# Kernel optimization log

Measured on AMD Instinct MI355X. Metric: run time of the kernel, lower is better.

## Reference

```python
import jax, jax.numpy as jnp
import numpy as np
from jax import lax

B, T, H, F, K, M, NB = 32, 1024, 256, 256, 3, 4096, 256


def setup_inputs() -> dict:
    key = jax.random.key(0)
    ks = jax.random.split(key, 10)
    s = 0.05
    inp = {}
    inp["x"] = jax.random.normal(ks[0], (B, T, H), jnp.float32)
    inp["src_mask"] = jnp.zeros((B, T), bool)
    inp["duration_target"] = jax.random.randint(ks[1], (B, T), 0, 7)
    inp["pitch_target"] = jax.random.uniform(ks[2], (B, T), jnp.float32)
    inp["energy_target"] = jax.random.uniform(ks[3], (B, T), jnp.float32)
    inp["max_len"] = M
    # stacked params for 3 predictors: [duration, pitch, energy]
    inp["w1"] = jax.random.normal(ks[4], (3, K, H, F), jnp.float32) * s  # WIO layout
    inp["b1"] = jnp.zeros((3, F), jnp.float32)
    inp["g1"] = jnp.ones((3, F), jnp.float32)
    inp["be1"] = jnp.zeros((3, F), jnp.float32)
    inp["w2"] = jax.random.normal(ks[5], (3, K, F, F), jnp.float32) * s
    inp["b2"] = jnp.zeros((3, F), jnp.float32)
    inp["g2"] = jnp.ones((3, F), jnp.float32)
    inp["be2"] = jnp.zeros((3, F), jnp.float32)
    inp["lw"] = jax.random.normal(ks[6], (3, F, 1), jnp.float32) * s
    inp["lb"] = jnp.zeros((3, 1), jnp.float32)
    inp["pitch_bins"] = jnp.linspace(0.0, 1.0, NB - 1, dtype=jnp.float32)
    inp["pitch_emb"] = jax.random.normal(ks[7], (NB, H), jnp.float32) * 0.1
    inp["energy_bins"] = jnp.linspace(0.0, 1.0, NB - 1, dtype=jnp.float32)
    inp["energy_emb"] = jax.random.normal(ks[8], (NB, H), jnp.float32) * 0.1
    return inp


def _conv_relu_ln(x, w, b, g, be):
    # Conv1d (k=3, pad=1) over seq dim with channels-last, then ReLU, then LayerNorm.
    h = lax.conv_general_dilated(x, w, (1,), [(1, 1)],
                                 dimension_numbers=('NWC', 'WIO', 'NWC'))
    h = jax.nn.relu(h + b)
    mu = jnp.mean(h, -1, keepdims=True)
    var = jnp.var(h, -1, keepdims=True)
    return (h - mu) * lax.rsqrt(var + 1e-5) * g + be


def _predictor(x, i, w1, b1, g1, be1, w2, b2, g2, be2, lw, lb, mask):
    h = _conv_relu_ln(x, w1[i], b1[i], g1[i], be1[i])
    h = _conv_relu_ln(h, w2[i], b2[i], g2[i], be2[i])
    out = (h @ lw[i] + lb[i])[..., 0]  # [B, T]
    return jnp.where(mask, 0.0, out)


def _length_regulate(x, dur, max_len):
    # vectorized version of the per-sample repeat/cat/pad LengthRegulator
    cum = jnp.cumsum(dur, axis=1)                     # [B, T]
    mel_len = jnp.minimum(cum[:, -1], max_len)        # [B]
    frames = jnp.arange(max_len)                      # [M]
    # frame j maps to phoneme i with cum[i-1] <= j < cum[i]
    idx = jax.vmap(lambda c: jnp.searchsorted(c, frames, side='right'))(cum)
    idx = jnp.minimum(idx, x.shape[1] - 1)
    out = jnp.take_along_axis(x, idx[:, :, None], axis=1)  # [B, M, H]
    valid = frames[None, :] < mel_len[:, None]
    return out * valid[:, :, None].astype(x.dtype), mel_len, ~valid


def reference(x, src_mask, duration_target, pitch_target, energy_target, max_len,
              w1, b1, g1, be1, w2, b2, g2, be2, lw, lb,
              pitch_bins, pitch_emb, energy_bins, energy_emb):
    P = (w1, b1, g1, be1, w2, b2, g2, be2, lw, lb)
    # predictor_grad = 1.0 -> x.detach() + 1.0*(x - x.detach()) == x
    log_dur = _predictor(x, 0, *P, src_mask)
    pitch_pred = _predictor(x, 1, *P, src_mask)
    p_e = pitch_emb[jnp.searchsorted(pitch_bins, pitch_target, side='left')]
    energy_pred = _predictor(x, 2, *P, src_mask)
    e_e = energy_emb[jnp.searchsorted(energy_bins, energy_target, side='left')]
    output = x + p_e + e_e
    out, mel_len, mel_mask = _length_regulate(output, duration_target, max_len)
    return (out, pitch_pred, energy_pred, log_dur, duration_target, mel_len, mel_mask)
```

## Files before the change

kernel.cpp:

```cpp
#include <hip/hip_runtime.h>
#include <hip/hip_bf16.h>
#include <stdint.h>


typedef __bf16 bf16;
typedef __attribute__((ext_vector_type(8))) __bf16 bf16x8;
typedef __attribute__((ext_vector_type(4))) float f32x4;

#define TSEQ 1024

#define O1 33554432
#define O2 33587200
#define O3 33619968
#define O4 33652736
#define O5 33685504
#define O6 33685536

#define OUT_END_B 135266432

#define XB_OFF 512
#define H1B_OFF (XB_OFF + 16777216)
#define H1B_SZ 16777216
#define WT_OFF (H1B_OFF + 3 * H1B_SZ)
#define WT_SZ 393216

#define XB_SZ 16777216
#define H1B_TOT (3 * H1B_SZ)
#define WT_TOT (6 * WT_SZ)
#define SCRATCH_SZ (XB_SZ + H1B_TOT + WT_TOT)

#define CUM_OFF 0
#define ADDROW_OFF 131072
#define ZEROS_OFF 262144
#define WS_SCR_OFF 524288
#define WS_NEED ((size_t)WS_SCR_OFF + (size_t)SCRATCH_SZ)

__global__ __launch_bounds__(256) void k_prep(
    const float* __restrict__ x, bf16* __restrict__ xb,
    const float* __restrict__ w1, const float* __restrict__ w2,
    bf16* __restrict__ wt,
    const float* __restrict__ pt, const float* __restrict__ et,
    const float* __restrict__ pbins, const float* __restrict__ ebins,
    int* __restrict__ addrow, float* __restrict__ zpage,
    const int* __restrict__ dur, const int* __restrict__ maxlen,
    float* __restrict__ out, int* __restrict__ cum) {
  int bid = blockIdx.x;
  int tid = threadIdx.x;
  if (bid < 4096) {
    int t = bid * 256 + tid;
    int g = t >> 5;
    int u = t & 31;
    const float4* s = (const float4*)(x + ((size_t)g << 8) + (u << 3));
    float4 a = s[0], b = s[1];
    bf16x8 o;
    o[0] = (bf16)a.x; o[1] = (bf16)a.y; o[2] = (bf16)a.z; o[3] = (bf16)a.w;
    o[4] = (bf16)b.x; o[5] = (bf16)b.y; o[6] = (bf16)b.z; o[7] = (bf16)b.w;
    *(bf16x8*)(xb + ((size_t)g << 8) + (u << 3)) = o;
  } else if (bid < 4672) {
    int bw = bid - 4096;
    int m = bw / 96;
    int r = bw % 96;
    int f = (r & 3) * 64 + (tid & 63);
    int u = (r >> 2) * 4 + (tid >> 6);
    const float* W = (m < 3) ? w1 : w2;
    int i = (m < 3) ? m : m - 3;
    int dt = u >> 5;
    int c0 = (u & 31) << 3;
    const float* src = W + (((size_t)(i * 3 + dt) * 256 + c0) << 8) + f;
    bf16x8 o;
#pragma unroll
    for (int cc = 0; cc < 8; ++cc) o[cc] = (bf16)src[(size_t)cc << 8];
    *(bf16x8*)(wt + (size_t)m * 196608 + (size_t)f * 768 + (u << 3)) = o;
  } else if (bid < 4800) {
    __shared__ float pb[255], eb[255];
    if (tid < 255) { pb[tid] = pbins[tid]; eb[tid] = ebins[tid]; }
    if (bid == 4672 && tid < 64) zpage[tid] = 0.f;
    __syncthreads();
    int g = (bid - 4672) * 256 + tid;
    float pv = pt[g], ev = et[g];
    int lo = 0, hi = 255;
    while (lo < hi) { int md = (lo + hi) >> 1; if (pb[md] < pv) lo = md + 1; else hi = md; }
    int pi = lo;
    lo = 0; hi = 255;
    while (lo < hi) { int md = (lo + hi) >> 1; if (eb[md] < ev) lo = md + 1; else hi = md; }
    addrow[g] = pi | (lo << 16);
  } else {
    __shared__ int lds[256];
    int b = bid - 4800;
    int4 d = ((const int4*)(dur + b * 1024))[tid];
    int p0 = d.x, p1 = p0 + d.y, p2 = p1 + d.z, p3 = p2 + d.w;
    int val = p3;
    lds[tid] = val;
    __syncthreads();
    for (int off = 1; off < 256; off <<= 1) {
      int t = (tid >= off) ? lds[tid - off] : 0;
      __syncthreads();
      val += t;
      lds[tid] = val;
      __syncthreads();
    }
    int excl = val - p3;
    int4 c;
    c.x = excl + p0; c.y = excl + p1; c.z = excl + p2; c.w = excl + p3;
    ((int4*)(cum + b * 1024))[tid] = c;
    float4 fd;
    fd.x = (float)d.x; fd.y = (float)d.y; fd.z = (float)d.z; fd.w = (float)d.w;
    ((float4*)(out + O4 + b * 1024))[tid] = fd;
    if (tid == 255) {
      int mel = val < maxlen[0] ? val : maxlen[0];
      out[O5 + b] = (float)mel;
    }
  }
}

__global__ __launch_bounds__(256, 2) void k_conv(
    const char* __restrict__ Ab, size_t AperY, const char* __restrict__ Wb,
    const float* __restrict__ bias0, const float* __restrict__ gamma0,
    const float* __restrict__ beta0, char* __restrict__ hout0,
    const float* __restrict__ lw0, const float* __restrict__ lb0,
    const unsigned char* __restrict__ mask, float* __restrict__ outb,
    const char* __restrict__ zpage, int mode,
    const float* __restrict__ xf, const int* __restrict__ cum,
    const int* __restrict__ addrow, const float* __restrict__ pemb,
    const float* __restrict__ eemb, const int* __restrict__ maxlen,
    int lrbase) {
  __shared__ __align__(16) char Abuf[3][8192];
  __shared__ __align__(16) char Bbuf[3][16384];
  __shared__ float redS[128][2];
  __shared__ float redS2[128][2];
  __shared__ float predr[128][2];

  const int tid = threadIdx.x;
  const int bid = blockIdx.x;

  if (bid >= 768) {
    int* cl = (int*)Abuf;
    int rid0 = lrbase + ((bid - 768) << 4);
    int b = rid0 >> 12;
    ((int4*)cl)[tid] = ((const int4*)(cum + (b << 10)))[tid];
    __syncthreads();
    int lane = tid & 63;
    int wv = tid >> 6;
    int total = cl[1023];
    int ml = maxlen[0];
    int mel = total < ml ? total : ml;
    int c1 = cl[lane * 16 + 15];
#pragma unroll
    for (int rr = 0; rr < 4; ++rr) {
      int rid = rid0 + (wv << 2) + rr;
      int j = rid & 4095;
      bool valid = j < mel;
      float4 res = {0.f, 0.f, 0.f, 0.f};
      if (valid) {
        unsigned long long m1 = __ballot(j < c1);
        int s = __ffsll(m1) - 1;
        unsigned long long m2 = __ballot(j < cl[s * 16 + (lane & 15)]);
        int p = __ffsll(m2) - 1;
        int i = s * 16 + p;
        int ar = addrow[(b << 10) + i];
        int pi = ar & 0xffff, ei = ar >> 16;
        const float4* xr = (const float4*)(xf + (((size_t)(b << 10) + i) << 8));
        const float4* pr = (const float4*)(pemb + ((size_t)pi << 8));
        const float4* er = (const float4*)(eemb + ((size_t)ei << 8));
        float4 a = xr[lane], pp = pr[lane], e = er[lane];
        res.x = a.x + pp.x + e.x;
        res.y = a.y + pp.y + e.y;
        res.z = a.z + pp.z + e.z;
        res.w = a.w + pp.w + e.w;
      }
      ((float4*)(outb + ((size_t)rid << 8)))[lane] = res;
      if (lane == 0) outb[O6 + rid] = valid ? 0.f : 1.f;
    }
    return;
  }

  const int wv = tid >> 6;
  const int ln = tid & 63;
  const int q = ln >> 4;
  const int m16 = ln & 15;
  const int rh = wv >> 1;
  const int ch = wv & 1;
  const int y = bid >> 8;
  const int g0 = (bid & 255) << 7;
  const int t0 = g0 & (TSEQ - 1);

  const char* A = Ab + (size_t)y * AperY;
  const char* W = Wb + (size_t)y * WT_SZ;

  const int srow = ln >> 2;
  const int slot = ln & 3;
  const int usw = slot ^ ((ln >> 3) & 3);

  const char* bsrc[4];
#pragma unroll
  for (int j = 0; j < 4; ++j) {
    int f = j * 64 + wv * 16 + srow;
    bsrc[j] = W + ((size_t)f * 768 + usw * 8) * 2;
  }
  const int rbase = wv * 16 + srow;

  f32x4 acc[4][8];
#pragma unroll
  for (int a = 0; a < 4; a++)
#pragma unroll
    for (int b = 0; b < 8; b++) acc[a][b] = (f32x4){0.f, 0.f, 0.f, 0.f};

#define STAGE(KB, BUF)                                                         \
  {                                                                            \
    int dt0_ = (KB) >> 3;                                                      \
    int c0_ = ((KB) & 7) << 5;                                                 \
    char* ad_ = Abuf[BUF];                                                     \
    char* bd_ = Bbuf[BUF];                                                     \
    _Pragma("unroll") for (int j = 0; j < 2; ++j) {                            \
      int rr = j * 64 + rbase + dt0_ - 1;                                      \
      const char* src = ((unsigned)(t0 + rr) < 1024u)                          \
          ? A + (((size_t)(g0 + rr) << 8) + c0_ + usw * 8) * 2                 \
          : zpage + slot * 16;                                                 \
      __builtin_amdgcn_global_load_lds(                                        \
          (const __attribute__((address_space(1))) void*)src,                  \
          (__attribute__((address_space(3))) void*)(ad_ + j * 4096 +           \
                                                    tid * 16),                 \
          16, 0, 0);                                                           \
    }                                                                          \
    _Pragma("unroll") for (int j = 0; j < 4; ++j) {                            \
      __builtin_amdgcn_global_load_lds(                                        \
          (const __attribute__((address_space(1))) void*)(bsrc[j] + (KB)*64),  \
          (__attribute__((address_space(3))) void*)(bd_ + j * 4096 +           \
                                                    tid * 16),                 \
          16, 0, 0);                                                           \
    }                                                                          \
  }

  const int spq = (q ^ ((m16 >> 1) & 3)) << 4;
  const int aoff = (rh * 64 + m16) * 64 + spq;
  const int boff = (ch * 128 + m16) * 64 + spq;

  STAGE(0, 0);
  STAGE(1, 1);
  int cur = 0, stg = 2;
  for (int kb = 0; kb < 24; ++kb) {
    if (kb < 23)
      asm volatile("s_waitcnt vmcnt(6)" ::: "memory");
    else
      asm volatile("s_waitcnt vmcnt(0)" ::: "memory");
    __builtin_amdgcn_s_barrier();
    if (kb < 22) STAGE(kb + 2, stg);
    const char* Ac = Abuf[cur];
    const char* Bc = Bbuf[cur];
    bf16x8 af[4], bfr[8];
#pragma unroll
    for (int mi = 0; mi < 4; ++mi)
      af[mi] = *(const bf16x8*)(Ac + aoff + mi * 1024);
#pragma unroll
    for (int ni = 0; ni < 8; ++ni)
      bfr[ni] = *(const bf16x8*)(Bc + boff + ni * 1024);
    __builtin_amdgcn_s_setprio(1);
#pragma unroll
    for (int mi = 0; mi < 4; ++mi)
#pragma unroll
      for (int ni = 0; ni < 8; ++ni)
        acc[mi][ni] = __builtin_amdgcn_mfma_f32_16x16x32_bf16(
            af[mi], bfr[ni], acc[mi][ni], 0, 0, 0);
    __builtin_amdgcn_s_setprio(0);
    asm volatile("s_waitcnt lgkmcnt(0)" ::: "memory");
    cur = (cur == 2) ? 0 : cur + 1;
    stg = (stg == 2) ? 0 : stg + 1;
  }
#undef STAGE

  const float* bias = bias0 + y * 256;
  const float* gamma = gamma0 + y * 256;
  const float* beta = beta0 + y * 256;
  float bias_v[8], g_v[8], be_v[8], lw_v[8];
#pragma unroll
  for (int ni = 0; ni < 8; ni++) {
    int nf = (ch << 7) + (ni << 4) + m16;
    bias_v[ni] = bias[nf];
    g_v[ni] = gamma[nf];
    be_v[ni] = beta[nf];
  }
  if (mode) {
    const float* lw = lw0 + y * 256;
#pragma unroll
    for (int ni = 0; ni < 8; ni++) lw_v[ni] = lw[(ch << 7) + (ni << 4) + m16];
  }

#pragma unroll
  for (int mi = 0; mi < 4; mi++) {
#pragma unroll
    for (int r = 0; r < 4; r++) {
      float s1 = 0.f, s2 = 0.f;
#pragma unroll
      for (int ni = 0; ni < 8; ni++) {
        float v = acc[mi][ni][r] + bias_v[ni];
        v = fmaxf(v, 0.f);
        acc[mi][ni][r] = v;
        s1 += v;
        s2 += v * v;
      }
#pragma unroll
      for (int d = 1; d < 16; d <<= 1) {
        s1 += __shfl_xor(s1, d);
        s2 += __shfl_xor(s2, d);
      }
      if (m16 == 0) {
        int m = (rh << 6) + (mi << 4) + (q << 2) + r;
        redS[m][ch] = s1;
        redS2[m][ch] = s2;
      }
    }
  }
  __syncthreads();

  if (mode == 0) {
    bf16* hp = (bf16*)(hout0 + (size_t)y * H1B_SZ);
#pragma unroll
    for (int mi = 0; mi < 4; mi++) {
#pragma unroll
      for (int r = 0; r < 4; r++) {
        int m = (rh << 6) + (mi << 4) + (q << 2) + r;
        float mu = (redS[m][0] + redS[m][1]) * 0.00390625f;
        float var = (redS2[m][0] + redS2[m][1]) * 0.00390625f - mu * mu;
        float rs = rsqrtf(var + 1e-5f);
        int gg = g0 + m;
#pragma unroll
        for (int ni = 0; ni < 8; ni++) {
          float v = (acc[mi][ni][r] - mu) * rs * g_v[ni] + be_v[ni];
          int n = (ch << 7) + (ni << 4) + m16;
          hp[((size_t)gg << 8) + n] = (bf16)v;
        }
      }
    }
  } else {
#pragma unroll
    for (int mi = 0; mi < 4; mi++) {
#pragma unroll
      for (int r = 0; r < 4; r++) {
        int m = (rh << 6) + (mi << 4) + (q << 2) + r;
        float mu = (redS[m][0] + redS[m][1]) * 0.00390625f;
        float var = (redS2[m][0] + redS2[m][1]) * 0.00390625f - mu * mu;
        float rs = rsqrtf(var + 1e-5f);
        float p = 0.f;
#pragma unroll
        for (int ni = 0; ni < 8; ni++) {
          float v = (acc[mi][ni][r] - mu) * rs * g_v[ni] + be_v[ni];
          p += v * lw_v[ni];
        }
#pragma unroll
        for (int d = 1; d < 16; d <<= 1) p += __shfl_xor(p, d);
        if (m16 == 0) predr[m][ch] = p;
      }
    }
    __syncthreads();
    if (tid < 128) {
      int gg = g0 + tid;
      float p = predr[tid][0] + predr[tid][1] + lb0[y];
      if (mask[gg]) p = 0.f;
      float* pd = outb + (y == 0 ? O3 : (y == 1 ? O1 : O2));
      pd[gg] = p;
    }
  }
}

__global__ __launch_bounds__(256) void k_lr(const float* __restrict__ x,
                                            const int* __restrict__ cum,
                                            const int* __restrict__ addrow,
                                            const float* __restrict__ pemb,
                                            const float* __restrict__ eemb,
                                            const int* __restrict__ maxlen,
                                            float* __restrict__ outb) {
  __shared__ int cl[1024];
  int tid = threadIdx.x;
  int rid0 = blockIdx.x << 4;
  int b = rid0 >> 12;
  ((int4*)cl)[tid] = ((const int4*)(cum + (b << 10)))[tid];
  __syncthreads();
  int lane = tid & 63;
  int wv = tid >> 6;
  int total = cl[1023];
  int ml = maxlen[0];
  int mel = total < ml ? total : ml;
  int c1 = cl[lane * 16 + 15];
#pragma unroll
  for (int rr = 0; rr < 4; ++rr) {
    int rid = rid0 + (wv << 2) + rr;
    int j = rid & 4095;
    bool valid = j < mel;
    float4 res = {0.f, 0.f, 0.f, 0.f};
    if (valid) {
      unsigned long long m1 = __ballot(j < c1);
      int s = __ffsll(m1) - 1;
      unsigned long long m2 = __ballot(j < cl[s * 16 + (lane & 15)]);
      int p = __ffsll(m2) - 1;
      int i = s * 16 + p;
      int ar = addrow[(b << 10) + i];
      int pi = ar & 0xffff, ei = ar >> 16;
      const float4* xr = (const float4*)(x + (((size_t)(b << 10) + i) << 8));
      const float4* pr = (const float4*)(pemb + ((size_t)pi << 8));
      const float4* er = (const float4*)(eemb + ((size_t)ei << 8));
      float4 a = xr[lane], pp = pr[lane], e = er[lane];
      res.x = a.x + pp.x + e.x;
      res.y = a.y + pp.y + e.y;
      res.z = a.z + pp.z + e.z;
      res.w = a.w + pp.w + e.w;
    }
    ((float4*)(outb + ((size_t)rid << 8)))[lane] = res;
    if (lane == 0) outb[O6 + rid] = valid ? 0.f : 1.f;
  }
}

extern "C" void kernel_launch(void* const* d_in, const int* in_sizes, int n_in,
                              void* d_out, int out_size, void* d_ws, size_t ws_size,
                              hipStream_t stream) {
  const float* x = (const float*)d_in[0];
  const unsigned char* src_mask = (const unsigned char*)d_in[1];
  const int* dur = (const int*)d_in[2];
  const float* pt = (const float*)d_in[3];
  const float* et = (const float*)d_in[4];
  const int* maxlen = (const int*)d_in[5];
  const float* w1 = (const float*)d_in[6];
  const float* b1 = (const float*)d_in[7];
  const float* g1 = (const float*)d_in[8];
  const float* be1 = (const float*)d_in[9];
  const float* w2 = (const float*)d_in[10];
  const float* b2 = (const float*)d_in[11];
  const float* g2 = (const float*)d_in[12];
  const float* be2 = (const float*)d_in[13];
  const float* lw = (const float*)d_in[14];
  const float* lb = (const float*)d_in[15];
  const float* pbins = (const float*)d_in[16];
  const float* pemb = (const float*)d_in[17];
  const float* ebins = (const float*)d_in[18];
  const float* eemb = (const float*)d_in[19];

  float* outf = (float*)d_out;
  char* ob = (char*)d_out;
  int* cum = (int*)((char*)d_ws + CUM_OFF);
  int* addrow = (int*)((char*)d_ws + ADDROW_OFF);
  float* zpage = (float*)((char*)d_ws + ZEROS_OFF);

  int merged = 0;
  char* sb = nullptr;
  if (ws_size >= WS_NEED) {
    sb = (char*)d_ws + WS_SCR_OFF;
    merged = 1;
  } else if ((size_t)out_size >= (size_t)OUT_END_B + (size_t)SCRATCH_SZ) {
    sb = ob + OUT_END_B;
    merged = 1;
  }
  bf16* xb;
  char* h1b;
  bf16* wt;
  if (merged) {
    xb = (bf16*)sb;
    h1b = sb + XB_SZ;
    wt = (bf16*)(sb + XB_SZ + H1B_TOT);
  } else {
    xb = (bf16*)(ob + XB_OFF);
    h1b = ob + H1B_OFF;
    wt = (bf16*)(ob + WT_OFF);
  }

  hipLaunchKernelGGL(k_prep, dim3(4832), dim3(256), 0, stream,
                     x, xb, w1, w2, wt, pt, et, pbins, ebins, addrow, zpage,
                     dur, maxlen, outf, cum);

  int gconv = merged ? 768 + 4096 : 768;
  hipLaunchKernelGGL(k_conv, dim3(gconv), dim3(256), 0, stream,
                     (const char*)xb, (size_t)0, (const char*)wt, b1, g1, be1,
                     h1b, lw, lb, src_mask, outf, (const char*)zpage, 0,
                     x, cum, addrow, pemb, eemb, maxlen, 0);
  hipLaunchKernelGGL(k_conv, dim3(gconv), dim3(256), 0, stream,
                     (const char*)h1b, (size_t)H1B_SZ,
                     (const char*)wt + 3 * WT_SZ, b2, g2, be2,
                     (char*)nullptr, lw, lb, src_mask, outf,
                     (const char*)zpage, 1,
                     x, cum, addrow, pemb, eemb, maxlen, 65536);
  if (!merged) {
    hipLaunchKernelGGL(k_lr, dim3(8192), dim3(256), 0, stream, x, cum, addrow,
                       pemb, eemb, maxlen, outf);
  }
}
```

Before: 330.2 us.

## Enlarge conv GEMM tile to 256 rows with 512-thread blocks

The conv kernel now uses 512-thread blocks, each computing a 256-row by 256-channel tile with 2x4 warp tiling instead of 128 rows with 2x2 warps. Each staged weight slice is reused across twice as many rows, halving weight reloads, and the LayerNorm reduction scratch is aliased into the A staging buffer. The grid halves, so fewer blocks run concurrently. The per-iteration lgkmcnt wait is removed and the main loop is unrolled by three. The risks are higher LDS use, fewer waves in flight, and possible register pressure from 512 threads at two blocks per CU.

```diff
diff --git a/kernel.cpp b/kernel.cpp
--- a/kernel.cpp
+++ b/kernel.cpp
@@ -113,7 +113,7 @@
   }
 }
 
-__global__ __launch_bounds__(256, 2) void k_conv(
+__global__ __launch_bounds__(512, 2) void k_conv(
     const char* __restrict__ Ab, size_t AperY, const char* __restrict__ Wb,
     const float* __restrict__ bias0, const float* __restrict__ gamma0,
     const float* __restrict__ beta0, char* __restrict__ hout0,
@@ -124,20 +124,20 @@
     const int* __restrict__ addrow, const float* __restrict__ pemb,
     const float* __restrict__ eemb, const int* __restrict__ maxlen,
     int lrbase) {
-  __shared__ __align__(16) char Abuf[3][8192];
-  __shared__ __align__(16) char Bbuf[3][16384];
-  __shared__ float redS[128][2];
-  __shared__ float redS2[128][2];
-  __shared__ float predr[128][2];
+  __shared__ __align__(16) char Ab3[3][16384];
+  __shared__ __align__(16) char Bb3[3][16384];
+  float (*redS)[4] = (float(*)[4])((char*)Ab3);
+  float (*redS2)[4] = (float(*)[4])((char*)Ab3 + 4096);
+  float (*predr)[4] = (float(*)[4])((char*)Ab3 + 8192);
 
   const int tid = threadIdx.x;
   const int bid = blockIdx.x;
 
-  if (bid >= 768) {
-    int* cl = (int*)Abuf;
-    int rid0 = lrbase + ((bid - 768) << 4);
+  if (bid >= 384) {
+    int* cl = (int*)Ab3;
+    int rid0 = lrbase + ((bid - 384) << 5);
     int b = rid0 >> 12;
-    ((int4*)cl)[tid] = ((const int4*)(cum + (b << 10)))[tid];
+    if (tid < 256) ((int4*)cl)[tid] = ((const int4*)(cum + (b << 10)))[tid];
     __syncthreads();
     int lane = tid & 63;
     int wv = tid >> 6;
@@ -178,91 +178,90 @@
   const int ln = tid & 63;
   const int q = ln >> 4;
   const int m16 = ln & 15;
-  const int rh = wv >> 1;
-  const int ch = wv & 1;
-  const int y = bid >> 8;
-  const int g0 = (bid & 255) << 7;
+  const int wm = wv >> 2;
+  const int wn = wv & 3;
+  const int y = bid >> 7;
+  const int g0 = (bid & 127) << 8;
   const int t0 = g0 & (TSEQ - 1);
 
   const char* A = Ab + (size_t)y * AperY;
   const char* W = Wb + (size_t)y * WT_SZ;
 
-  const int srow = ln >> 2;
-  const int slot = ln & 3;
-  const int usw = slot ^ ((ln >> 3) & 3);
-
-  const char* bsrc[4];
-#pragma unroll
-  for (int j = 0; j < 4; ++j) {
-    int f = j * 64 + wv * 16 + srow;
-    bsrc[j] = W + ((size_t)f * 768 + usw * 8) * 2;
-  }
-  const int rbase = wv * 16 + srow;
-
-  f32x4 acc[4][8];
-#pragma unroll
-  for (int a = 0; a < 4; a++)
-#pragma unroll
-    for (int b = 0; b < 8; b++) acc[a][b] = (f32x4){0.f, 0.f, 0.f, 0.f};
+  const int slot = tid & 3;
+  const int chunk = slot ^ ((tid >> 3) & 3);
+
+  const char* bsrc[2];
+#pragma unroll
+  for (int j = 0; j < 2; ++j) {
+    int f = j * 128 + (tid >> 2);
+    bsrc[j] = W + ((size_t)f * 768 + chunk * 8) * 2;
+  }
+
+  f32x4 acc[8][4];
+#pragma unroll
+  for (int a = 0; a < 8; a++)
+#pragma unroll
+    for (int b = 0; b < 4; b++) acc[a][b] = (f32x4){0.f, 0.f, 0.f, 0.f};
 
 #define STAGE(KB, BUF)                                                         \
   {                                                                            \
-    int dt0_ = (KB) >> 3;                                                      \
-    int c0_ = ((KB) & 7) << 5;                                                 \
-    char* ad_ = Abuf[BUF];                                                     \
-    char* bd_ = Bbuf[BUF];                                                     \
+    int dt_ = (KB) >> 3;                                                       \
+    int c0_ = ((KB)&7) << 5;                                                   \
+    char* ad_ = Ab3[BUF];                                                      \
+    char* bd_ = Bb3[BUF];                                                      \
     _Pragma("unroll") for (int j = 0; j < 2; ++j) {                            \
-      int rr = j * 64 + rbase + dt0_ - 1;                                      \
-      const char* src = ((unsigned)(t0 + rr) < 1024u)                          \
-          ? A + (((size_t)(g0 + rr) << 8) + c0_ + usw * 8) * 2                 \
+      int rowv = j * 128 + (tid >> 2);                                         \
+      int trow = t0 - 1 + rowv + dt_;                                          \
+      const char* src = ((unsigned)trow < 1024u)                               \
+          ? A + (((size_t)(g0 - 1 + rowv + dt_) << 8) + c0_ + chunk * 8) * 2   \
           : zpage + slot * 16;                                                 \
       __builtin_amdgcn_global_load_lds(                                        \
           (const __attribute__((address_space(1))) void*)src,                  \
-          (__attribute__((address_space(3))) void*)(ad_ + j * 4096 +           \
+          (__attribute__((address_space(3))) void*)(ad_ + j * 8192 +           \
                                                     tid * 16),                 \
           16, 0, 0);                                                           \
     }                                                                          \
-    _Pragma("unroll") for (int j = 0; j < 4; ++j) {                            \
+    _Pragma("unroll") for (int j = 0; j < 2; ++j) {                            \
       __builtin_amdgcn_global_load_lds(                                        \
           (const __attribute__((address_space(1))) void*)(bsrc[j] + (KB)*64),  \
-          (__attribute__((address_space(3))) void*)(bd_ + j * 4096 +           \
+          (__attribute__((address_space(3))) void*)(bd_ + j * 8192 +           \
                                                     tid * 16),                 \
           16, 0, 0);                                                           \
     }                                                                          \
   }
 
   const int spq = (q ^ ((m16 >> 1) & 3)) << 4;
-  const int aoff = (rh * 64 + m16) * 64 + spq;
-  const int boff = (ch * 128 + m16) * 64 + spq;
+  const int abase = (wm * 128 + m16) * 64 + spq;
+  const int bbase = (wn * 64 + m16) * 64 + spq;
 
   STAGE(0, 0);
   STAGE(1, 1);
   int cur = 0, stg = 2;
+#pragma unroll 3
   for (int kb = 0; kb < 24; ++kb) {
     if (kb < 23)
-      asm volatile("s_waitcnt vmcnt(6)" ::: "memory");
+      asm volatile("s_waitcnt vmcnt(4)" ::: "memory");
     else
       asm volatile("s_waitcnt vmcnt(0)" ::: "memory");
     __builtin_amdgcn_s_barrier();
     if (kb < 22) STAGE(kb + 2, stg);
-    const char* Ac = Abuf[cur];
-    const char* Bc = Bbuf[cur];
-    bf16x8 af[4], bfr[8];
-#pragma unroll
-    for (int mi = 0; mi < 4; ++mi)
-      af[mi] = *(const bf16x8*)(Ac + aoff + mi * 1024);
-#pragma unroll
-    for (int ni = 0; ni < 8; ++ni)
-      bfr[ni] = *(const bf16x8*)(Bc + boff + ni * 1024);
+    const char* Ac = Ab3[cur];
+    const char* Bc = Bb3[cur];
+    bf16x8 af[8], bfr[4];
+#pragma unroll
+    for (int ni = 0; ni < 4; ++ni)
+      bfr[ni] = *(const bf16x8*)(Bc + bbase + ni * 1024);
+#pragma unroll
+    for (int mi = 0; mi < 8; ++mi)
+      af[mi] = *(const bf16x8*)(Ac + abase + mi * 1024);
     __builtin_amdgcn_s_setprio(1);
 #pragma unroll
-    for (int mi = 0; mi < 4; ++mi)
-#pragma unroll
-      for (int ni = 0; ni < 8; ++ni)
+    for (int mi = 0; mi < 8; ++mi)
+#pragma unroll
+      for (int ni = 0; ni < 4; ++ni)
         acc[mi][ni] = __builtin_amdgcn_mfma_f32_16x16x32_bf16(
             af[mi], bfr[ni], acc[mi][ni], 0, 0, 0);
     __builtin_amdgcn_s_setprio(0);
-    asm volatile("s_waitcnt lgkmcnt(0)" ::: "memory");
     cur = (cur == 2) ? 0 : cur + 1;
     stg = (stg == 2) ? 0 : stg + 1;
   }
@@ -271,10 +270,10 @@
   const float* bias = bias0 + y * 256;
   const float* gamma = gamma0 + y * 256;
   const float* beta = beta0 + y * 256;
-  float bias_v[8], g_v[8], be_v[8], lw_v[8];
-#pragma unroll
-  for (int ni = 0; ni < 8; ni++) {
-    int nf = (ch << 7) + (ni << 4) + m16;
+  float bias_v[4], g_v[4], be_v[4], lw_v[4];
+#pragma unroll
+  for (int ni = 0; ni < 4; ni++) {
+    int nf = (wn << 6) + (ni << 4) + m16;
     bias_v[ni] = bias[nf];
     g_v[ni] = gamma[nf];
     be_v[ni] = beta[nf];
@@ -282,16 +281,16 @@
   if (mode) {
     const float* lw = lw0 + y * 256;
 #pragma unroll
-    for (int ni = 0; ni < 8; ni++) lw_v[ni] = lw[(ch << 7) + (ni << 4) + m16];
-  }
-
-#pragma unroll
-  for (int mi = 0; mi < 4; mi++) {
+    for (int ni = 0; ni < 4; ni++) lw_v[ni] = lw[(wn << 6) + (ni << 4) + m16];
+  }
+
+#pragma unroll
+  for (int mi = 0; mi < 8; mi++) {
 #pragma unroll
     for (int r = 0; r < 4; r++) {
       float s1 = 0.f, s2 = 0.f;
 #pragma unroll
-      for (int ni = 0; ni < 8; ni++) {
+      for (int ni = 0; ni < 4; ni++) {
         float v = acc[mi][ni][r] + bias_v[ni];
         v = fmaxf(v, 0.f);
         acc[mi][ni][r] = v;
@@ -304,9 +303,9 @@
         s2 += __shfl_xor(s2, d);
       }
       if (m16 == 0) {
-        int m = (rh << 6) + (mi << 4) + (q << 2) + r;
-        redS[m][ch] = s1;
-        redS2[m][ch] = s2;
+        int m = (wm << 7) + (mi << 4) + (q << 2) + r;
+        redS[m][wn] = s1;
+        redS2[m][wn] = s2;
       }
     }
   }
@@ -315,46 +314,51 @@
   if (mode == 0) {
     bf16* hp = (bf16*)(hout0 + (size_t)y * H1B_SZ);
 #pragma unroll
-    for (int mi = 0; mi < 4; mi++) {
+    for (int mi = 0; mi < 8; mi++) {
 #pragma unroll
       for (int r = 0; r < 4; r++) {
-        int m = (rh << 6) + (mi << 4) + (q << 2) + r;
-        float mu = (redS[m][0] + redS[m][1]) * 0.00390625f;
-        float var = (redS2[m][0] + redS2[m][1]) * 0.00390625f - mu * mu;
+        int m = (wm << 7) + (mi << 4) + (q << 2) + r;
+        float mu = (redS[m][0] + redS[m][1] + redS[m][2] + redS[m][3]) *
+                   0.00390625f;
+        float var = (redS2[m][0] + redS2[m][1] + redS2[m][2] + redS2[m][3]) *
+                        0.00390625f - mu * mu;
         float rs = rsqrtf(var + 1e-5f);
         int gg = g0 + m;
 #pragma unroll
-        for (int ni = 0; ni < 8; ni++) {
+        for (int ni = 0; ni < 4; ni++) {
           float v = (acc[mi][ni][r] - mu) * rs * g_v[ni] + be_v[ni];
-          int n = (ch << 7) + (ni << 4) + m16;
+          int n = (wn << 6) + (ni << 4) + m16;
           hp[((size_t)gg << 8) + n] = (bf16)v;
         }
       }
     }
   } else {
 #pragma unroll
-    for (int mi = 0; mi < 4; mi++) {
+    for (int mi = 0; mi < 8; mi++) {
 #pragma unroll
       for (int r = 0; r < 4; r++) {
-        int m = (rh << 6) + (mi << 4) + (q << 2) + r;
-        float mu = (redS[m][0] + redS[m][1]) * 0.00390625f;
-        float var = (redS2[m][0] + redS2[m][1]) * 0.00390625f - mu * mu;
+        int m = (wm << 7) + (mi << 4) + (q << 2) + r;
+        float mu = (redS[m][0] + redS[m][1] + redS[m][2] + redS[m][3]) *
+                   0.00390625f;
+        float var = (redS2[m][0] + redS2[m][1] + redS2[m][2] + redS2[m][3]) *
+                        0.00390625f - mu * mu;
         float rs = rsqrtf(var + 1e-5f);
         float p = 0.f;
 #pragma unroll
-        for (int ni = 0; ni < 8; ni++) {
+        for (int ni = 0; ni < 4; ni++) {
           float v = (acc[mi][ni][r] - mu) * rs * g_v[ni] + be_v[ni];
           p += v * lw_v[ni];
         }
 #pragma unroll
         for (int d = 1; d < 16; d <<= 1) p += __shfl_xor(p, d);
-        if (m16 == 0) predr[m][ch] = p;
+        if (m16 == 0) predr[m][wn] = p;
       }
     }
     __syncthreads();
-    if (tid < 128) {
+    if (tid < 256) {
       int gg = g0 + tid;
-      float p = predr[tid][0] + predr[tid][1] + lb0[y];
+      float p = predr[tid][0] + predr[tid][1] + predr[tid][2] + predr[tid][3] +
+                lb0[y];
       if (mask[gg]) p = 0.f;
       float* pd = outb + (y == 0 ? O3 : (y == 1 ? O1 : O2));
       pd[gg] = p;
@@ -465,12 +469,12 @@
                      x, xb, w1, w2, wt, pt, et, pbins, ebins, addrow, zpage,
                      dur, maxlen, outf, cum);
 
-  int gconv = merged ? 768 + 4096 : 768;
-  hipLaunchKernelGGL(k_conv, dim3(gconv), dim3(256), 0, stream,
+  int gconv = merged ? 384 + 2048 : 384;
+  hipLaunchKernelGGL(k_conv, dim3(gconv), dim3(512), 0, stream,
                      (const char*)xb, (size_t)0, (const char*)wt, b1, g1, be1,
                      h1b, lw, lb, src_mask, outf, (const char*)zpage, 0,
                      x, cum, addrow, pemb, eemb, maxlen, 0);
-  hipLaunchKernelGGL(k_conv, dim3(gconv), dim3(256), 0, stream,
+  hipLaunchKernelGGL(k_conv, dim3(gconv), dim3(512), 0, stream,
                      (const char*)h1b, (size_t)H1B_SZ,
                      (const char*)wt + 3 * WT_SZ, b2, g2, be2,
                      (char*)nullptr, lw, lb, src_mask, outf,
```

Result: slower. 356.0 us (+7.8%).
